# Kernel optimization log

Measured on AMD Instinct MI355X. Metric: run time of the kernel, lower is better.

## Reference

```python
import jax, jax.numpy as jnp
import numpy as np

D = 768       # GATv2 in/out feats (num_heads=1)
D_OUT = 384   # fc output
K = 51        # round(top_rate * L) = round(0.1 * 512)
EPS = 1e-5    # nn.LayerNorm default eps


def _layer_norm(x, g, b):
    mu = jnp.mean(x, axis=-1, keepdims=True)
    var = jnp.mean((x - mu) ** 2, axis=-1, keepdims=True)
    return (x - mu) / jnp.sqrt(var + EPS) * g + b


def setup_inputs() -> dict:
    key = jax.random.key(0)
    ks = jax.random.split(key, 12)
    B, L = 4, 512
    s = 0.02
    return {
        "hidden_state": jax.random.normal(ks[0], (B, L, D), jnp.float32),
        "attention": jax.random.uniform(ks[1], (B, L, L), jnp.float32),
        # GATv2Conv params (fc_src, fc_dst, attn vector, output bias)
        "W_src": jax.random.normal(ks[2], (D, D), jnp.float32) * s,
        "b_src": jnp.zeros((D,), jnp.float32),
        "W_dst": jax.random.normal(ks[3], (D, D), jnp.float32) * s,
        "b_dst": jnp.zeros((D,), jnp.float32),
        "attn_vec": jax.random.normal(ks[4], (D,), jnp.float32) * s,
        "gat_bias": jnp.zeros((D,), jnp.float32),
        # GlobalAttentionPooling gate_nn: Linear(768, 1)
        "gate_W": jax.random.normal(ks[5], (D, 1), jnp.float32) * s,
        "gate_b": jnp.zeros((1,), jnp.float32),
        # LayerNorm(768)
        "ln_g": jnp.ones((D,), jnp.float32),
        "ln_b": jnp.zeros((D,), jnp.float32),
        # fc: Linear(768, 384)
        "fc_W": jax.random.normal(ks[6], (D, D_OUT), jnp.float32) * s,
        "fc_b": jnp.zeros((D_OUT,), jnp.float32),
        # LayerNorm(384)
        "ln2_g": jnp.ones((D_OUT,), jnp.float32),
        "ln2_b": jnp.zeros((D_OUT,), jnp.float32),
        "mask": jnp.ones((B, L), jnp.int32),  # unused by the original forward
        "type": 0,                              # unused string/type flag
    }


def reference(hidden_state, attention, W_src, b_src, W_dst, b_dst, attn_vec,
              gat_bias, gate_W, gate_b, ln_g, ln_b, fc_W, fc_b, ln2_g, ln2_b,
              mask, type):
    B, L, _ = hidden_state.shape
    # --- topk sparsification: each node i keeps K source neighbors ---
    vals, idx = jax.lax.top_k(attention, K)          # [B, L, K]
    valid = vals > 0.0                                # edges kept by pos_sign filter

    # --- GATv2Conv (num_heads=1, residual=Identity since 768==768) ---
    feat_src = hidden_state @ W_src + b_src           # [B, L, D]
    feat_dst = hidden_state @ W_dst + b_dst           # [B, L, D]
    g = feat_src[jnp.arange(B)[:, None, None], idx]   # [B, L, K, D] gathered src feats
    e = jax.nn.leaky_relu(g + feat_dst[:, :, None, :], 0.2)
    scores = jnp.einsum("blkd,d->blk", e, attn_vec)   # [B, L, K]
    scores = jnp.where(valid, scores, -1e9)           # removed edges masked out
    a = jax.nn.softmax(scores, axis=-1)               # edge_softmax per dst node
    h = jnp.einsum("blk,blkd->bld", a, g)             # weighted scatter-sum
    h = h + hidden_state + gat_bias                   # residual (identity) + bias
    h = jax.nn.leaky_relu(h, 0.01)                    # nn.LeakyReLU activation

    # --- GlobalAttentionPooling: softmax(gate) weighted segment reduce ---
    gate = h @ gate_W + gate_b                        # [B, L, 1]
    p = jax.nn.softmax(gate, axis=1)
    pooled = jnp.sum(p * h, axis=1)                   # [B, D]

    # --- head: fc(dropout(ln(relu(out)))) then ln2 (dropout = eval identity) ---
    out = _layer_norm(jax.nn.relu(pooled), ln_g, ln_b)
    out = out @ fc_W + fc_b
    out = _layer_norm(out, ln2_g, ln2_b)
    return out
```

## Files before the change

kernel.cpp:

```cpp
#include <hip/hip_runtime.h>
#include <math.h>

#define D 768
#define DOUT 384
#define LSEQ 512
#define BATCH 4
#define KTOP 51
#define EPS 1e-5f

typedef unsigned short ushort_t;
typedef __bf16 bf16x8 __attribute__((ext_vector_type(8)));
typedef float f32x4 __attribute__((ext_vector_type(4)));

#define GLOAD16(gp, lp)                                                        \
    __builtin_amdgcn_global_load_lds(                                          \
        (const __attribute__((address_space(1))) unsigned int*)(gp),           \
        (__attribute__((address_space(3))) unsigned int*)(lp), 16, 0, 0)

__device__ __forceinline__ ushort_t f2bf(float f) {
    unsigned int u = __builtin_bit_cast(unsigned int, f);
    u = (u + 0x7FFFu + ((u >> 16) & 1u)) >> 16;
    return (ushort_t)u;
}

__device__ __forceinline__ float bf2f(ushort_t u) {
    unsigned int v = ((unsigned int)u) << 16;
    return __builtin_bit_cast(float, v);
}

__global__ __launch_bounds__(256) void prep_kernel(const float* __restrict__ hidden,
                                                   ushort_t* __restrict__ Ah,
                                                   const float* __restrict__ W0,
                                                   const float* __restrict__ W1,
                                                   ushort_t* __restrict__ WT0,
                                                   ushort_t* __restrict__ WT1,
                                                   float* __restrict__ pooled,
                                                   float* __restrict__ z) {
    __shared__ float tile[32][33];
    const int bid = blockIdx.x;
    const int tid = threadIdx.x;
    if (bid < 1536) {
        const int i = (bid * 256 + tid) * 4;
        const float4 v = *(const float4*)(hidden + i);
        ushort4 o;
        o.x = f2bf(v.x); o.y = f2bf(v.y); o.z = f2bf(v.z); o.w = f2bf(v.w);
        *(ushort4*)(Ah + i) = o;
    } else if (bid < 2688) {
        const int t = bid - 1536;
        const int zz = t / 576;
        const int rem = t - zz * 576;
        const int by = rem / 24, bx = rem - by * 24;
        const float* W = zz ? W1 : W0;
        ushort_t* WT = zz ? WT1 : WT0;
        const int kbase = by * 32;
        const int nbase = bx * 32;
        const int r = tid >> 3, c4 = (tid & 7) * 4;

        const float4 v = *(const float4*)(W + (size_t)(kbase + r) * D + nbase + c4);
        tile[r][c4 + 0] = v.x; tile[r][c4 + 1] = v.y;
        tile[r][c4 + 2] = v.z; tile[r][c4 + 3] = v.w;
        __syncthreads();
        ushort4 o;
        o.x = f2bf(tile[c4 + 0][r]); o.y = f2bf(tile[c4 + 1][r]);
        o.z = f2bf(tile[c4 + 2][r]); o.w = f2bf(tile[c4 + 3][r]);
        *(ushort4*)(WT + (size_t)(nbase + r) * D + kbase + c4) = o;
    } else {
        for (int i = tid; i < BATCH * D; i += 256) pooled[i] = 0.f;
        for (int i = tid; i < BATCH * DOUT; i += 256) z[i] = 0.f;
    }
}

__global__ __launch_bounds__(256) void feat_gemm_kernel(const ushort_t* __restrict__ Ah,
                                                        const ushort_t* __restrict__ WT0,
                                                        const float* __restrict__ b0,
                                                        ushort_t* __restrict__ Csrc_bf,
                                                        const ushort_t* __restrict__ WT1,
                                                        const float* __restrict__ b1,
                                                        float* __restrict__ Cdst) {
    const int bid = blockIdx.x;
    const int wid = (bid & 7) * 96 + (bid >> 3);
    const int zz = wid / 384;
    const int rem = wid - zz * 384;
    const int tileY = rem / 12;
    const int tileX = rem - tileY * 12;

    const ushort_t* WT = zz ? WT1 : WT0;
    const float* bias = zz ? b1 : b0;

    __shared__ ushort_t As[64 * 64];
    __shared__ ushort_t Bs[64 * 64];

    const int tid = threadIdx.x;
    const int lane = tid & 63;
    const int wave = tid >> 6;
    const int quad = lane >> 4;
    const int m15 = lane & 15;
    const int qRow = (wave & 1) * 32;
    const int qCol = (wave >> 1) * 32;

    const int rowBase = tileY * 64;
    const int colBase = tileX * 64;

    const int e0 = tid * 8;
    const int r0 = e0 >> 6;
    const int c0 = e0 & 63;
    const int cc = c0 >> 3;
    const int csw = (cc ^ (r0 & 7)) << 3;
    const ushort_t* Abase = Ah + (size_t)rowBase * D;
    const ushort_t* Bbase = WT + (size_t)colBase * D;

    f32x4 acc[2][2] = {};

    for (int kk = 0; kk < D; kk += 64) {
        __syncthreads();
        GLOAD16(Abase + (size_t)r0 * D + kk + csw, &As[e0]);
        GLOAD16(Abase + (size_t)(r0 + 32) * D + kk + csw, &As[e0 + 2048]);
        GLOAD16(Bbase + (size_t)r0 * D + kk + csw, &Bs[e0]);
        GLOAD16(Bbase + (size_t)(r0 + 32) * D + kk + csw, &Bs[e0 + 2048]);
        __syncthreads();

        bf16x8 a[2][2], b[2][2];
#pragma unroll
        for (int i = 0; i < 2; ++i) {
            const int row = qRow + i * 16 + m15;
            const int sw = row & 7;
#pragma unroll
            for (int ks = 0; ks < 2; ++ks)
                a[i][ks] = *(const bf16x8*)&As[row * 64 + ((((ks << 2) + quad) ^ sw) << 3)];
        }
#pragma unroll
        for (int j = 0; j < 2; ++j) {
            const int row = qCol + j * 16 + m15;
            const int sw = row & 7;
#pragma unroll
            for (int ks = 0; ks < 2; ++ks)
                b[j][ks] = *(const bf16x8*)&Bs[row * 64 + ((((ks << 2) + quad) ^ sw) << 3)];
        }
#pragma unroll
        for (int ks = 0; ks < 2; ++ks)
#pragma unroll
            for (int i = 0; i < 2; ++i)
#pragma unroll
                for (int j = 0; j < 2; ++j)
                    acc[i][j] = __builtin_amdgcn_mfma_f32_16x16x32_bf16(a[i][ks], b[j][ks], acc[i][j], 0, 0, 0);
    }

    if (zz == 0) {
#pragma unroll
        for (int j = 0; j < 2; ++j) {
            const int col = colBase + qCol + j * 16 + m15;
            const float bv = bias[col];
#pragma unroll
            for (int i = 0; i < 2; ++i) {
                ushort_t* Cp = Csrc_bf + (size_t)(rowBase + qRow + i * 16 + quad * 4) * D + col;
#pragma unroll
                for (int r = 0; r < 4; ++r)
                    Cp[(size_t)r * D] = f2bf(acc[i][j][r] + bv);
            }
        }
    } else {
#pragma unroll
        for (int j = 0; j < 2; ++j) {
            const int col = colBase + qCol + j * 16 + m15;
            const float bv = bias[col];
#pragma unroll
            for (int i = 0; i < 2; ++i) {
                float* Cp = Cdst + (size_t)(rowBase + qRow + i * 16 + quad * 4) * D + col;
#pragma unroll
                for (int r = 0; r < 4; ++r)
                    Cp[(size_t)r * D] = acc[i][j][r] + bv;
            }
        }
    }
}

__global__ __launch_bounds__(256) void scoregath_kernel(const float* __restrict__ attn,
                                                        const ushort_t* __restrict__ fsrc_bf,
                                                        const float* __restrict__ feat_dst,
                                                        const float* __restrict__ attn_vec,
                                                        const float* __restrict__ gat_bias,
                                                        const float* __restrict__ hidden,
                                                        const float* __restrict__ gate_W,
                                                        const float* __restrict__ gate_b,
                                                        ushort_t* __restrict__ h,
                                                        float* __restrict__ gate) {
    const int bid = blockIdx.x;
    const int row = (bid & 7) * 256 + (bid >> 3);
    const int b = row >> 9;
    const int tid = threadIdx.x;
    const int lane = tid & 63;
    const int wave = tid >> 6;

    __shared__ float vals[LSEQ];
    __shared__ float cval[320];
    __shared__ int   cidx[320];
    __shared__ int   nhi, outSlot;
    __shared__ int   kid[KTOP];
    __shared__ float kvv[KTOP];
    __shared__ float wm[4], wl[4];
    __shared__ float hpart[4][D];
    __shared__ float gred[4];

    if (tid == 0) { nhi = 0; outSlot = 0; }

    const float* a = attn + (size_t)row * LSEQ;
    const float v0 = a[tid];
    const float v1 = a[tid + 256];
    vals[tid] = v0;
    vals[tid + 256] = v1;
    __syncthreads();

    if (v0 > 0.75f) {
        const int s = atomicAdd(&nhi, 1);
        if (s < 320) { cval[s] = v0; cidx[s] = tid; }
    }
    if (v1 > 0.75f) {
        const int s = atomicAdd(&nhi, 1);
        if (s < 320) { cval[s] = v1; cidx[s] = tid + 256; }
    }
    __syncthreads();

    const int n = nhi;
    if (n >= KTOP && n <= 320) {
        if (tid < n) {
            const float v = cval[tid];
            const int e = cidx[tid];
            int r = 0;
            for (int j = 0; j < n; ++j) {
                const float u = cval[j];
                r += (u > v) || (u == v && cidx[j] < e);
            }
            if (r < KTOP) {
                const int s = atomicAdd(&outSlot, 1);
                kid[s] = e; kvv[s] = v;
            }
        }
    } else {
#pragma unroll
        for (int e0 = 0; e0 < 2; ++e0) {
            const int e = tid + e0 * 256;
            const float v = vals[e];
            int r = 0;
            for (int j = 0; j < LSEQ; ++j) {
                const float u = vals[j];
                r += (u > v) || (u == v && j < e);
            }
            if (r < KTOP) {
                const int s = atomicAdd(&outSlot, 1);
                kid[s] = e; kvv[s] = v;
            }
        }
    }

    const int d0 = lane * 8;
    const int d1 = 512 + lane * 4;
    const float* fdp = feat_dst + (size_t)row * D;
    float fdr[12], avr[12];
    {
        const float4 f0 = *(const float4*)(fdp + d0);
        const float4 f1 = *(const float4*)(fdp + d0 + 4);
        const float4 f2 = *(const float4*)(fdp + d1);
        const float4 a0 = *(const float4*)(attn_vec + d0);
        const float4 a1 = *(const float4*)(attn_vec + d0 + 4);
        const float4 a2 = *(const float4*)(attn_vec + d1);
        fdr[0]=f0.x; fdr[1]=f0.y; fdr[2]=f0.z;  fdr[3]=f0.w;
        fdr[4]=f1.x; fdr[5]=f1.y; fdr[6]=f1.z;  fdr[7]=f1.w;
        fdr[8]=f2.x; fdr[9]=f2.y; fdr[10]=f2.z; fdr[11]=f2.w;
        avr[0]=a0.x; avr[1]=a0.y; avr[2]=a0.z;  avr[3]=a0.w;
        avr[4]=a1.x; avr[5]=a1.y; avr[6]=a1.z;  avr[7]=a1.w;
        avr[8]=a2.x; avr[9]=a2.y; avr[10]=a2.z; avr[11]=a2.w;
    }
    __syncthreads();

    const ushort_t* fb = fsrc_bf + ((size_t)(b << 9)) * D;
    float m_run = -3.0e38f, l_run = 0.f;
    float acc[12] = {};
    for (int k = wave; k < KTOP; k += 4) {
        const ushort_t* g = fb + (size_t)kid[k] * D;
        const bf16x8 g0 = *(const bf16x8*)(g + d0);
        const ushort4 g1 = *(const ushort4*)(g + d1);

        float gf[12];
#pragma unroll
        for (int jj = 0; jj < 8; ++jj) gf[jj] = (float)g0[jj];
        gf[8] = bf2f(g1.x); gf[9] = bf2f(g1.y);
        gf[10] = bf2f(g1.z); gf[11] = bf2f(g1.w);

        float s = 0.f;
#pragma unroll
        for (int jj = 0; jj < 12; ++jj) {
            float x = gf[jj] + fdr[jj];
            x = x > 0.f ? x : 0.2f * x;
            s += x * avr[jj];
        }
#pragma unroll
        for (int off = 32; off > 0; off >>= 1) s += __shfl_xor(s, off);
        s = (kvv[k] > 0.f) ? s : -1e9f;

        if (s > m_run + 8.f) {
            const float rs = __expf(m_run - s);
            l_run *= rs;
#pragma unroll
            for (int jj = 0; jj < 12; ++jj) acc[jj] *= rs;
            m_run = s;
        }
        const float p = __expf(s - m_run);
        l_run += p;
#pragma unroll
        for (int jj = 0; jj < 12; ++jj) acc[jj] += p * gf[jj];
    }

    if (lane == 0) { wm[wave] = m_run; wl[wave] = l_run; }
    *(float4*)&hpart[wave][d0]     = *(float4*)&acc[0];
    *(float4*)&hpart[wave][d0 + 4] = *(float4*)&acc[4];
    *(float4*)&hpart[wave][d1]     = *(float4*)&acc[8];
    __syncthreads();

    const float M = fmaxf(fmaxf(wm[0], wm[1]), fmaxf(wm[2], wm[3]));
    const float r0 = __expf(wm[0] - M), r1 = __expf(wm[1] - M);
    const float r2 = __expf(wm[2] - M), r3 = __expf(wm[3] - M);
    const float invL = 1.f / (r0 * wl[0] + r1 * wl[1] + r2 * wl[2] + r3 * wl[3]);

    float dotp = 0.f;
    const float* hid = hidden + (size_t)row * D;
    ushort_t* hb = h + (size_t)row * D;
#pragma unroll
    for (int j = 0; j < 3; ++j) {
        const int d = tid + j * 256;
        const float hv = (r0 * hpart[0][d] + r1 * hpart[1][d] +
                          r2 * hpart[2][d] + r3 * hpart[3][d]) * invL;
        float v = hv + hid[d] + gat_bias[d];
        v = v > 0.f ? v : 0.01f * v;
        hb[d] = f2bf(v);
        dotp += v * gate_W[d];
    }
#pragma unroll
    for (int off = 32; off > 0; off >>= 1) dotp += __shfl_xor(dotp, off);
    if (lane == 0) gred[wave] = dotp;
    __syncthreads();
    if (tid == 0) gate[row] = gate_b[0] + gred[0] + gred[1] + gred[2] + gred[3];
}

__global__ __launch_bounds__(256) void pool_kernel(const ushort_t* __restrict__ h,
                                                   const float* __restrict__ gate,
                                                   float* __restrict__ pooled) {
    const int b = blockIdx.z;
    const int lbase = blockIdx.y * 64;
    const int d = blockIdx.x * 256 + threadIdx.x;
    const int tid = threadIdx.x;
    const int lane = tid & 63;
    const int w = tid >> 6;

    __shared__ float wred[4];
    __shared__ float ps[64];

    const float g0 = gate[b * LSEQ + tid];
    const float g1 = gate[b * LSEQ + tid + 256];
    float m = fmaxf(g0, g1);
#pragma unroll
    for (int off = 32; off > 0; off >>= 1) m = fmaxf(m, __shfl_xor(m, off));
    if (lane == 0) wred[w] = m;
    __syncthreads();
    m = fmaxf(fmaxf(wred[0], wred[1]), fmaxf(wred[2], wred[3]));
    float e = __expf(g0 - m) + __expf(g1 - m);
#pragma unroll
    for (int off = 32; off > 0; off >>= 1) e += __shfl_xor(e, off);
    __syncthreads();
    if (lane == 0) wred[w] = e;
    __syncthreads();
    const float inv = 1.f / (wred[0] + wred[1] + wred[2] + wred[3]);
    if (tid < 64) ps[tid] = __expf(gate[b * LSEQ + lbase + tid] - m) * inv;
    __syncthreads();

    const ushort_t* hb = h + ((size_t)(b * LSEQ + lbase)) * D + d;
    float acc = 0.f;
#pragma unroll 8
    for (int l = 0; l < 64; ++l) {
        acc += ps[l] * bf2f(hb[(size_t)l * D]);
    }
    atomicAdd(&pooled[b * D + d], acc);
}

__global__ __launch_bounds__(256) void fc_kernel(const float* __restrict__ pooled,
                                                 const float* __restrict__ ln_g,
                                                 const float* __restrict__ ln_b,
                                                 const float* __restrict__ fc_W,
                                                 float* __restrict__ z) {
    const int b = blockIdx.z;
    const int by = blockIdx.y;
    const int dbase = by * 256;
    const int jbase = blockIdx.x * 64;
    const int tid = threadIdx.x;
    const int lane = tid & 63;
    const int w = tid >> 6;
    const int jt = tid & 63;
    const int sub = tid >> 6;

    __shared__ float wred[4];
    __shared__ float ys[256];
    __shared__ float part[4][64];

    float v[3];
#pragma unroll
    for (int i = 0; i < 3; ++i) v[i] = fmaxf(pooled[b * D + tid + i * 256], 0.f);

    float s = v[0] + v[1] + v[2];
#pragma unroll
    for (int off = 32; off > 0; off >>= 1) s += __shfl_xor(s, off);
    if (lane == 0) wred[w] = s;
    __syncthreads();
    const float mu = (wred[0] + wred[1] + wred[2] + wred[3]) / (float)D;
    float vs = 0.f;
#pragma unroll
    for (int i = 0; i < 3; ++i) { const float dd = v[i] - mu; vs += dd * dd; }
#pragma unroll
    for (int off = 32; off > 0; off >>= 1) vs += __shfl_xor(vs, off);
    __syncthreads();
    if (lane == 0) wred[w] = vs;
    __syncthreads();
    const float rstd = rsqrtf((wred[0] + wred[1] + wred[2] + wred[3]) / (float)D + EPS);

    const float vb = (by == 0) ? v[0] : (by == 1 ? v[1] : v[2]);
    ys[tid] = (vb - mu) * rstd * ln_g[dbase + tid] + ln_b[dbase + tid];
    __syncthreads();

    const float* W = fc_W + (size_t)(dbase + sub * 64) * DOUT + jbase + jt;
    const float* yy = ys + sub * 64;
    float acc = 0.f;
#pragma unroll 8
    for (int i = 0; i < 64; ++i) {
        acc += yy[i] * W[(size_t)i * DOUT];
    }
    part[sub][jt] = acc;
    __syncthreads();
    if (sub == 0) {
        const float tot = part[0][jt] + part[1][jt] + part[2][jt] + part[3][jt];
        atomicAdd(&z[b * DOUT + jbase + jt], tot);
    }
}

__global__ __launch_bounds__(384) void ln2_kernel(const float* __restrict__ z,
                                                  const float* __restrict__ fc_b,
                                                  const float* __restrict__ ln2_g,
                                                  const float* __restrict__ ln2_b,
                                                  float* __restrict__ out) {
    const int b = blockIdx.x;
    const int tid = threadIdx.x;
    const int lane = tid & 63;
    const int wave = tid >> 6;
    __shared__ float wred[6];

    const float v = z[b * DOUT + tid] + fc_b[tid];

    float s = v;
#pragma unroll
    for (int off = 32; off > 0; off >>= 1) s += __shfl_xor(s, off);
    if (lane == 0) wred[wave] = s;
    __syncthreads();
    float mu = 0.f;
#pragma unroll
    for (int w = 0; w < 6; ++w) mu += wred[w];
    mu /= (float)DOUT;
    __syncthreads();

    const float dd = v - mu;
    float s2 = dd * dd;
#pragma unroll
    for (int off = 32; off > 0; off >>= 1) s2 += __shfl_xor(s2, off);
    if (lane == 0) wred[wave] = s2;
    __syncthreads();
    float var = 0.f;
#pragma unroll
    for (int w = 0; w < 6; ++w) var += wred[w];
    const float rstd = rsqrtf(var / (float)DOUT + EPS);

    out[b * DOUT + tid] = dd * rstd * ln2_g[tid] + ln2_b[tid];
}

extern "C" void kernel_launch(void* const* d_in, const int* in_sizes, int n_in,
                              void* d_out, int out_size, void* d_ws, size_t ws_size,
                              hipStream_t stream) {
    const float* hidden   = (const float*)d_in[0];
    const float* attention= (const float*)d_in[1];
    const float* W_src    = (const float*)d_in[2];
    const float* b_src    = (const float*)d_in[3];
    const float* W_dst    = (const float*)d_in[4];
    const float* b_dst    = (const float*)d_in[5];
    const float* attn_vec = (const float*)d_in[6];
    const float* gat_bias = (const float*)d_in[7];
    const float* gate_W   = (const float*)d_in[8];
    const float* gate_b   = (const float*)d_in[9];
    const float* ln_g     = (const float*)d_in[10];
    const float* ln_b     = (const float*)d_in[11];
    const float* fc_W     = (const float*)d_in[12];
    const float* fc_b     = (const float*)d_in[13];
    const float* ln2_g    = (const float*)d_in[14];
    const float* ln2_b    = (const float*)d_in[15];
    float* out = (float*)d_out;

    const int M = BATCH * LSEQ;
    float* feat_dst = (float*)d_ws;
    float* gate     = feat_dst + (size_t)M * D;
    float* pooled   = gate + M;
    float* z        = pooled + BATCH * D;
    ushort_t* Ah    = (ushort_t*)(z + BATCH * DOUT);
    ushort_t* WT0   = Ah + (size_t)M * D;
    ushort_t* WT1   = WT0 + (size_t)D * D;
    ushort_t* fsrcb = WT1 + (size_t)D * D;
    ushort_t* h     = fsrcb + (size_t)M * D;

    hipLaunchKernelGGL(prep_kernel, dim3(2689), dim3(256), 0, stream,
                       hidden, Ah, W_src, W_dst, WT0, WT1, pooled, z);
    hipLaunchKernelGGL(feat_gemm_kernel, dim3(768), dim3(256), 0, stream,
                       Ah, WT0, b_src, fsrcb, WT1, b_dst, feat_dst);
    hipLaunchKernelGGL(scoregath_kernel, dim3(M), dim3(256), 0, stream,
                       attention, fsrcb, feat_dst, attn_vec, gat_bias, hidden,
                       gate_W, gate_b, h, gate);
    hipLaunchKernelGGL(pool_kernel, dim3(D / 256, LSEQ / 64, BATCH), dim3(256), 0, stream,
                       h, gate, pooled);
    hipLaunchKernelGGL(fc_kernel, dim3(DOUT / 64, D / 256, BATCH), dim3(256), 0, stream,
                       pooled, ln_g, ln_b, fc_W, z);
    hipLaunchKernelGGL(ln2_kernel, dim3(BATCH), dim3(384), 0, stream,
                       z, fc_b, ln2_g, ln2_b, out);
}
```

Baseline: 152.6 us.

## Use wave-aggregated atomics, packed f32x2 math, and prefetch next gathered row

Replaces per-thread LDS atomics in the top-k candidate compaction and selection with wave-level ballot/popcount aggregation, so each wave issues one atomic. The per-edge GATv2 score and accumulation loop now uses two-wide float vectors to allow packed FMA instructions, and leaky ReLU is written as a max. The gathered source row for the next iteration is loaded one step ahead so global latency overlaps compute. Costs are extra registers for the prefetch buffer and one redundant load on the final iteration.

```diff
diff --git a/kernel.cpp b/kernel.cpp
--- a/kernel.cpp
+++ b/kernel.cpp
@@ -11,6 +11,7 @@
 typedef unsigned short ushort_t;
 typedef __bf16 bf16x8 __attribute__((ext_vector_type(8)));
 typedef float f32x4 __attribute__((ext_vector_type(4)));
+typedef float f32x2 __attribute__((ext_vector_type(2)));
 
 #define GLOAD16(gp, lp)                                                        \
     __builtin_amdgcn_global_load_lds(                                          \
@@ -210,13 +211,23 @@
     vals[tid + 256] = v1;
     __syncthreads();
 
-    if (v0 > 0.75f) {
-        const int s = atomicAdd(&nhi, 1);
-        if (s < 320) { cval[s] = v0; cidx[s] = tid; }
-    }
-    if (v1 > 0.75f) {
-        const int s = atomicAdd(&nhi, 1);
-        if (s < 320) { cval[s] = v1; cidx[s] = tid + 256; }
+    {
+        const unsigned long long m0 = __ballot(v0 > 0.75f);
+        const unsigned long long m1 = __ballot(v1 > 0.75f);
+        const int c0 = __popcll(m0);
+        const int c1 = __popcll(m1);
+        int base = 0;
+        if (lane == 0) base = atomicAdd(&nhi, c0 + c1);
+        base = __shfl(base, 0);
+        const unsigned long long below = (1ull << lane) - 1ull;
+        if (v0 > 0.75f) {
+            const int s = base + __popcll(m0 & below);
+            if (s < 320) { cval[s] = v0; cidx[s] = tid; }
+        }
+        if (v1 > 0.75f) {
+            const int s = base + c0 + __popcll(m1 & below);
+            if (s < 320) { cval[s] = v1; cidx[s] = tid + 256; }
+        }
     }
     __syncthreads();
 
@@ -230,9 +241,18 @@
                 const float u = cval[j];
                 r += (u > v) || (u == v && cidx[j] < e);
             }
-            if (r < KTOP) {
-                const int s = atomicAdd(&outSlot, 1);
-                kid[s] = e; kvv[s] = v;
+            const bool keep = (r < KTOP);
+            const unsigned long long mk = __ballot(keep);
+            const int cnt = __popcll(mk);
+            if (cnt > 0) {
+                const int leader = __ffsll((unsigned long long)mk) - 1;
+                int base = 0;
+                if (lane == leader) base = atomicAdd(&outSlot, cnt);
+                base = __shfl(base, leader);
+                if (keep) {
+                    const int s = base + __popcll(mk & ((1ull << lane) - 1ull));
+                    kid[s] = e; kvv[s] = v;
+                }
             }
         }
     } else {
@@ -255,7 +275,7 @@
     const int d0 = lane * 8;
     const int d1 = 512 + lane * 4;
     const float* fdp = feat_dst + (size_t)row * D;
-    float fdr[12], avr[12];
+    f32x2 fdr[6], avr[6];
     {
         const float4 f0 = *(const float4*)(fdp + d0);
         const float4 f1 = *(const float4*)(fdp + d0 + 4);
@@ -263,36 +283,45 @@
         const float4 a0 = *(const float4*)(attn_vec + d0);
         const float4 a1 = *(const float4*)(attn_vec + d0 + 4);
         const float4 a2 = *(const float4*)(attn_vec + d1);
-        fdr[0]=f0.x; fdr[1]=f0.y; fdr[2]=f0.z;  fdr[3]=f0.w;
-        fdr[4]=f1.x; fdr[5]=f1.y; fdr[6]=f1.z;  fdr[7]=f1.w;
-        fdr[8]=f2.x; fdr[9]=f2.y; fdr[10]=f2.z; fdr[11]=f2.w;
-        avr[0]=a0.x; avr[1]=a0.y; avr[2]=a0.z;  avr[3]=a0.w;
-        avr[4]=a1.x; avr[5]=a1.y; avr[6]=a1.z;  avr[7]=a1.w;
-        avr[8]=a2.x; avr[9]=a2.y; avr[10]=a2.z; avr[11]=a2.w;
+        fdr[0] = f32x2{f0.x, f0.y}; fdr[1] = f32x2{f0.z, f0.w};
+        fdr[2] = f32x2{f1.x, f1.y}; fdr[3] = f32x2{f1.z, f1.w};
+        fdr[4] = f32x2{f2.x, f2.y}; fdr[5] = f32x2{f2.z, f2.w};
+        avr[0] = f32x2{a0.x, a0.y}; avr[1] = f32x2{a0.z, a0.w};
+        avr[2] = f32x2{a1.x, a1.y}; avr[3] = f32x2{a1.z, a1.w};
+        avr[4] = f32x2{a2.x, a2.y}; avr[5] = f32x2{a2.z, a2.w};
     }
     __syncthreads();
 
     const ushort_t* fb = fsrc_bf + ((size_t)(b << 9)) * D;
     float m_run = -3.0e38f, l_run = 0.f;
-    float acc[12] = {};
+    f32x2 acc[6] = {};
+
+    const ushort_t* gp0 = fb + (size_t)kid[wave] * D;
+    bf16x8 cg0 = *(const bf16x8*)(gp0 + d0);
+    ushort4 cg1 = *(const ushort4*)(gp0 + d1);
+
     for (int k = wave; k < KTOP; k += 4) {
-        const ushort_t* g = fb + (size_t)kid[k] * D;
-        const bf16x8 g0 = *(const bf16x8*)(g + d0);
-        const ushort4 g1 = *(const ushort4*)(g + d1);
-
-        float gf[12];
-#pragma unroll
-        for (int jj = 0; jj < 8; ++jj) gf[jj] = (float)g0[jj];
-        gf[8] = bf2f(g1.x); gf[9] = bf2f(g1.y);
-        gf[10] = bf2f(g1.z); gf[11] = bf2f(g1.w);
-
-        float s = 0.f;
-#pragma unroll
-        for (int jj = 0; jj < 12; ++jj) {
-            float x = gf[jj] + fdr[jj];
-            x = x > 0.f ? x : 0.2f * x;
-            s += x * avr[jj];
-        }
+        const int kn = (k + 4 < KTOP) ? (k + 4) : k;
+        const ushort_t* gn = fb + (size_t)kid[kn] * D;
+        const bf16x8 ng0 = *(const bf16x8*)(gn + d0);
+        const ushort4 ng1 = *(const ushort4*)(gn + d1);
+
+        f32x2 gf[6];
+        gf[0] = f32x2{(float)cg0[0], (float)cg0[1]};
+        gf[1] = f32x2{(float)cg0[2], (float)cg0[3]};
+        gf[2] = f32x2{(float)cg0[4], (float)cg0[5]};
+        gf[3] = f32x2{(float)cg0[6], (float)cg0[7]};
+        gf[4] = f32x2{bf2f(cg1.x), bf2f(cg1.y)};
+        gf[5] = f32x2{bf2f(cg1.z), bf2f(cg1.w)};
+
+        f32x2 s2 = {0.f, 0.f};
+#pragma unroll
+        for (int jj = 0; jj < 6; ++jj) {
+            f32x2 x = gf[jj] + fdr[jj];
+            x = __builtin_elementwise_max(x, x * 0.2f);
+            s2 += x * avr[jj];
+        }
+        float s = s2.x + s2.y;
 #pragma unroll
         for (int off = 32; off > 0; off >>= 1) s += __shfl_xor(s, off);
         s = (kvv[k] > 0.f) ? s : -1e9f;
@@ -301,19 +330,24 @@
             const float rs = __expf(m_run - s);
             l_run *= rs;
 #pragma unroll
-            for (int jj = 0; jj < 12; ++jj) acc[jj] *= rs;
+            for (int jj = 0; jj < 6; ++jj) acc[jj] *= rs;
             m_run = s;
         }
         const float p = __expf(s - m_run);
         l_run += p;
 #pragma unroll
-        for (int jj = 0; jj < 12; ++jj) acc[jj] += p * gf[jj];
+        for (int jj = 0; jj < 6; ++jj) acc[jj] += p * gf[jj];
+
+        cg0 = ng0; cg1 = ng1;
     }
 
     if (lane == 0) { wm[wave] = m_run; wl[wave] = l_run; }
-    *(float4*)&hpart[wave][d0]     = *(float4*)&acc[0];
-    *(float4*)&hpart[wave][d0 + 4] = *(float4*)&acc[4];
-    *(float4*)&hpart[wave][d1]     = *(float4*)&acc[8];
+    *(f32x2*)&hpart[wave][d0]     = acc[0];
+    *(f32x2*)&hpart[wave][d0 + 2] = acc[1];
+    *(f32x2*)&hpart[wave][d0 + 4] = acc[2];
+    *(f32x2*)&hpart[wave][d0 + 6] = acc[3];
+    *(f32x2*)&hpart[wave][d1]     = acc[4];
+    *(f32x2*)&hpart[wave][d1 + 2] = acc[5];
     __syncthreads();
 
     const float M = fmaxf(fmaxf(wm[0], wm[1]), fmaxf(wm[2], wm[3]));
```

Result: no change. 151.3 us (-0.9%).
